# Performance work log

Measured on AMD Instinct MI355X. Metric: run time of the kernel, lower is better.

The kernel has to match this reference:

```python
import jax, jax.numpy as jnp
import numpy as np

B, N = 16, 1024
NT = 3            # atom types
NPT = 6           # pair types = NT*(NT+1)//2


def setup_inputs() -> dict:
    key = jax.random.key(0)
    ks = jax.random.split(key, 8)
    types = jax.random.randint(ks[0], (B, N), 0, NT, dtype=jnp.int32)
    n_atoms = jax.random.randint(ks[1], (B,), N // 2, N + 1, dtype=jnp.int32)
    # interatomic distances in a physically plausible range [1.5, 5.5)
    distances = 1.5 + 4.0 * jax.random.uniform(ks[2], (B, N, N), dtype=jnp.float32)
    # pair type index from (ti, tj) using combinations_with_replacement ordering
    ti = types[:, :, None]
    tj = types[:, None, :]
    lo = jnp.minimum(ti, tj)
    hi = jnp.maximum(ti, tj)
    pair_types = (lo * (2 * NT - lo + 1) // 2 + (hi - lo)).astype(jnp.int32)
    # per-pair-type potential params [a, b, r0] and density params [xi, q, r0]
    phi_params = jnp.stack([
        0.5 + jax.random.uniform(ks[3], (NPT,)),          # a
        1.0 + jax.random.uniform(ks[4], (NPT,)),          # b
        2.0 + jax.random.uniform(ks[5], (NPT,)),          # r0
    ], axis=-1).astype(jnp.float32)
    rho_params = jnp.stack([
        0.5 + jax.random.uniform(ks[6], (NPT,)),          # xi
        1.0 + jax.random.uniform(ks[7], (NPT,)),          # q
        2.0 + jax.random.uniform(jax.random.fold_in(key, 9), (NPT,)),  # r0
    ], axis=-1).astype(jnp.float32)
    emb_params = jnp.stack([
        0.5 + jax.random.uniform(jax.random.fold_in(key, 10), (NT,)),  # A (sqrt embedding)
        0.1 * jax.random.normal(jax.random.fold_in(key, 11), (NT,)),   # offset
    ], axis=-1).astype(jnp.float32)
    return {"types": types, "n_atoms": n_atoms, "distances": distances,
            "pair_types": pair_types, "phi_params": phi_params,
            "rho_params": rho_params, "emb_params": emb_params}


def reference(types, n_atoms, distances, pair_types, phi_params, rho_params, emb_params):
    # masks emulating raggedness: valid atoms and valid (i != j) pairs
    idx = jnp.arange(N)
    atom_mask = idx[None, :] < n_atoms[:, None]                      # [B, N]
    pair_mask = (atom_mask[:, :, None] & atom_mask[:, None, :]
                 & ~jnp.eye(N, dtype=bool)[None])                    # [B, N, N]

    # per-pair-type routed potential and density (branchless 'where' method)
    pp = phi_params[pair_types]                                      # [B, N, N, 3]
    phi = pp[..., 0] * jnp.exp(-pp[..., 1] * (distances - pp[..., 2]))
    rp = rho_params[pair_types]
    rho = rp[..., 0] * jnp.exp(-rp[..., 1] * (distances - rp[..., 2]))
    phi = jnp.where(pair_mask, phi, 0.0)
    rho = jnp.where(pair_mask, rho, 0.0)

    # scatter/reduce over neighbors -> per-atom quantities
    sum_rho = jnp.sum(rho * rho, axis=-1)                            # [B, N]
    sum_phi = jnp.sum(phi, axis=-1)                                  # [B, N]
    sum_rho = jnp.maximum(sum_rho, 1e-30)

    # per-atom-type embedding F(|x|) + offset
    A = emb_params[types, 0]
    off = emb_params[types, 1]
    emb = -A * jnp.sqrt(jnp.abs(sum_rho)) + off

    atomic_energies = jnp.where(atom_mask, sum_phi + emb, 0.0)       # [B, N]
    energy = jnp.sum(atomic_energies, axis=-1, keepdims=True)        # [B, 1]
    energy_per_atom = energy / n_atoms[:, None].astype(energy.dtype)
    return energy_per_atom
```

## Files before the change

### kernel.cpp

```cpp
#include <hip/hip_runtime.h>

#define NN 1024
#define BB 16
#define NTY 3

__global__ __launch_bounds__(256) void eam_rows(
    const int* __restrict__ types, const int* __restrict__ n_atoms,
    const float* __restrict__ distances,
    const float* __restrict__ phi_params, const float* __restrict__ rho_params,
    const float* __restrict__ emb_params, float* __restrict__ blk_part)
{
    __shared__ int4   s_types4[NN / 4];
    __shared__ float4 s_tbl[NTY * NTY];
    __shared__ float  s_rowe[8];

    const int tid = threadIdx.x;
    const int b  = blockIdx.y;
    const int bx = blockIdx.x;

    s_types4[tid] = ((const int4*)(types + b * NN))[tid];

    if (tid < NTY * NTY) {
        const int ti = tid / NTY, tj = tid % NTY;
        const int lo = min(ti, tj), hi = max(ti, tj);
        const int pt = lo * (2 * NTY - lo + 1) / 2 + (hi - lo);
        const float p0 = phi_params[pt * 3 + 0];
        const float p1 = phi_params[pt * 3 + 1];
        const float p2 = phi_params[pt * 3 + 2];
        const float r0 = rho_params[pt * 3 + 0];
        const float r1 = rho_params[pt * 3 + 1];
        const float r2 = rho_params[pt * 3 + 2];
        const float LOG2E = 1.44269504088896f;
        const float ra = r0 * __expf(r1 * r2);
        s_tbl[tid] = make_float4(p0 * __expf(p1 * p2), -p1 * LOG2E,
                                 ra * ra, -2.0f * r1 * LOG2E);
    }
    __syncthreads();

    const int lane = tid & 63;
    const int wave = tid >> 6;
    const int na = n_atoms[b];
    const bool p2 = na > 512;
    const bool p3 = na > 768;
    const int* s_types = (const int*)s_types4;

#pragma unroll
    for (int rr = 0; rr < 2; ++rr) {
        const int i = bx + (wave * 2 + rr) * 128;
        float rowE = 0.f;
        if (i < na) {
            const int ti = s_types[i];
            const float4* drow =
                (const float4*)(distances + ((size_t)(b * NN + i)) * NN);
            float4 v0 = drow[lane];
            float4 v1 = drow[64 + lane];
            float4 v2 = make_float4(0.f, 0.f, 0.f, 0.f);
            float4 v3 = make_float4(0.f, 0.f, 0.f, 0.f);
            if (p2) v2 = drow[128 + lane];
            if (p3) v3 = drow[192 + lane];

            float sph = 0.f, srh = 0.f;

#define EAM_EL(E, DD, TT, JB)                                                 \
            {                                                                 \
                const float4 prm = s_tbl[ti * NTY + (TT)];                    \
                float phi  = prm.x * __builtin_amdgcn_exp2f(prm.y * (DD));    \
                float rho2 = prm.z * __builtin_amdgcn_exp2f(prm.w * (DD));    \
                const int j = (JB) + (E);                                     \
                if (j >= na || j == i) { phi = 0.f; rho2 = 0.f; }             \
                sph += phi;                                                   \
                srh += rho2;                                                  \
            }
#define EAM_PASS(P, V)                                                        \
            {                                                                 \
                const int c4 = (P) * 64 + lane;                               \
                const int4 tj4 = s_types4[c4];                                \
                const int jb = c4 * 4;                                        \
                EAM_EL(0, (V).x, tj4.x, jb)                                   \
                EAM_EL(1, (V).y, tj4.y, jb)                                   \
                EAM_EL(2, (V).z, tj4.z, jb)                                   \
                EAM_EL(3, (V).w, tj4.w, jb)                                   \
            }
            EAM_PASS(0, v0)
            EAM_PASS(1, v1)
            if (p2) EAM_PASS(2, v2)
            if (p3) EAM_PASS(3, v3)
#undef EAM_PASS
#undef EAM_EL

#pragma unroll
            for (int o = 32; o > 0; o >>= 1) {
                sph += __shfl_xor(sph, o, 64);
                srh += __shfl_xor(srh, o, 64);
            }
            const float A   = emb_params[ti * 2 + 0];
            const float off = emb_params[ti * 2 + 1];
            rowE = sph + (-A * sqrtf(fmaxf(srh, 1e-30f)) + off);
        }
        if (lane == 0) s_rowe[wave * 2 + rr] = rowE;
    }
    __syncthreads();

    if (tid == 0) {
        float s = 0.f;
#pragma unroll
        for (int k = 0; k < 8; ++k) s += s_rowe[k];
        blk_part[b * 128 + bx] = s;
    }
}

__global__ __launch_bounds__(64) void eam_reduce(
    const float* __restrict__ blk_part, const int* __restrict__ n_atoms,
    float* __restrict__ out)
{
    const int b = blockIdx.x;
    const int lane = threadIdx.x;
    float s = blk_part[b * 128 + lane] + blk_part[b * 128 + 64 + lane];
#pragma unroll
    for (int o = 32; o > 0; o >>= 1) s += __shfl_xor(s, o, 64);
    if (lane == 0) out[b] = s / (float)n_atoms[b];
}

extern "C" void kernel_launch(void* const* d_in, const int* in_sizes, int n_in,
                              void* d_out, int out_size, void* d_ws, size_t ws_size,
                              hipStream_t stream) {
    const int*   types      = (const int*)d_in[0];
    const int*   n_atoms    = (const int*)d_in[1];
    const float* distances  = (const float*)d_in[2];
    const float* phi_params = (const float*)d_in[4];
    const float* rho_params = (const float*)d_in[5];
    const float* emb_params = (const float*)d_in[6];

    float* blk_part = (float*)d_ws;

    eam_rows<<<dim3(128, BB), 256, 0, stream>>>(
        types, n_atoms, distances, phi_params, rho_params, emb_params, blk_part);
    eam_reduce<<<BB, 64, 0, stream>>>(blk_part, n_atoms, (float*)d_out);
}
```

Measured before the change: 19.96 us.

## Fuse final reduction via atomics, interleave two rows, drop per-element diagonal mask

Removes the second reduce kernel by having each block atomically add its scaled partial sum into the output, which is zeroed with a memset first. Each wave now loads both of its rows up front and processes them together, so the loads overlap and the type-table lookup is shared. The per-element j==i check is replaced by subtracting the diagonal term at the end, and j>=na masking is applied only in the last pass. Risks include nondeterministic float atomic ordering, an added memset on the stream, and cancellation error from subtracting the diagonal term.

```diff
diff --git a/kernel.cpp b/kernel.cpp
--- a/kernel.cpp
+++ b/kernel.cpp
@@ -8,7 +8,7 @@
     const int* __restrict__ types, const int* __restrict__ n_atoms,
     const float* __restrict__ distances,
     const float* __restrict__ phi_params, const float* __restrict__ rho_params,
-    const float* __restrict__ emb_params, float* __restrict__ blk_part)
+    const float* __restrict__ emb_params, float* __restrict__ out)
 {
     __shared__ int4   s_types4[NN / 4];
     __shared__ float4 s_tbl[NTY * NTY];
@@ -44,60 +44,105 @@
     const bool p3 = na > 768;
     const int* s_types = (const int*)s_types4;
 
-#pragma unroll
-    for (int rr = 0; rr < 2; ++rr) {
-        const int i = bx + (wave * 2 + rr) * 128;
-        float rowE = 0.f;
-        if (i < na) {
-            const int ti = s_types[i];
-            const float4* drow =
-                (const float4*)(distances + ((size_t)(b * NN + i)) * NN);
-            float4 v0 = drow[lane];
-            float4 v1 = drow[64 + lane];
-            float4 v2 = make_float4(0.f, 0.f, 0.f, 0.f);
-            float4 v3 = make_float4(0.f, 0.f, 0.f, 0.f);
-            if (p2) v2 = drow[128 + lane];
-            if (p3) v3 = drow[192 + lane];
+    const int iA = bx + wave * 256;
+    const int iB = iA + 128;
+    const bool vA = iA < na;
+    const bool vB = iB < na;
 
-            float sph = 0.f, srh = 0.f;
+    const float4 z4 = make_float4(0.f, 0.f, 0.f, 0.f);
+    float4 a0 = z4, a1 = z4, a2 = z4, a3 = z4;
+    float4 b0 = z4, b1 = z4, b2 = z4, b3 = z4;
+    float dAii = 0.f, dBii = 0.f;
+    int tiA = 0, tiB = 0;
 
-#define EAM_EL(E, DD, TT, JB)                                                 \
-            {                                                                 \
-                const float4 prm = s_tbl[ti * NTY + (TT)];                    \
-                float phi  = prm.x * __builtin_amdgcn_exp2f(prm.y * (DD));    \
-                float rho2 = prm.z * __builtin_amdgcn_exp2f(prm.w * (DD));    \
-                const int j = (JB) + (E);                                     \
-                if (j >= na || j == i) { phi = 0.f; rho2 = 0.f; }             \
-                sph += phi;                                                   \
-                srh += rho2;                                                  \
-            }
-#define EAM_PASS(P, V)                                                        \
-            {                                                                 \
-                const int c4 = (P) * 64 + lane;                               \
-                const int4 tj4 = s_types4[c4];                                \
-                const int jb = c4 * 4;                                        \
-                EAM_EL(0, (V).x, tj4.x, jb)                                   \
-                EAM_EL(1, (V).y, tj4.y, jb)                                   \
-                EAM_EL(2, (V).z, tj4.z, jb)                                   \
-                EAM_EL(3, (V).w, tj4.w, jb)                                   \
-            }
-            EAM_PASS(0, v0)
-            EAM_PASS(1, v1)
-            if (p2) EAM_PASS(2, v2)
-            if (p3) EAM_PASS(3, v3)
+    if (vA) {
+        tiA = s_types[iA];
+        const float4* rA = (const float4*)(distances + ((size_t)(b * NN + iA)) * NN);
+        a0 = rA[lane];
+        a1 = rA[64 + lane];
+        if (p2) a2 = rA[128 + lane];
+        if (p3) a3 = rA[192 + lane];
+        dAii = ((const float*)rA)[iA];
+    }
+    if (vB) {
+        tiB = s_types[iB];
+        const float4* rB = (const float4*)(distances + ((size_t)(b * NN + iB)) * NN);
+        b0 = rB[lane];
+        b1 = rB[64 + lane];
+        if (p2) b2 = rB[128 + lane];
+        if (p3) b3 = rB[192 + lane];
+        dBii = ((const float*)rB)[iB];
+    }
+
+    float sphA = 0.f, srhA = 0.f, sphB = 0.f, srhB = 0.f;
+    const int tiA3 = tiA * NTY, tiB3 = tiB * NTY;
+
+#define EAM_EL(E, DA, DB, TT, MASKED, JB)                                     \
+    {                                                                         \
+        const int tj = (TT);                                                  \
+        const float4 pA = s_tbl[tiA3 + tj];                                   \
+        const float4 pB = s_tbl[tiB3 + tj];                                   \
+        float phA = pA.x * __builtin_amdgcn_exp2f(pA.y * (DA));               \
+        float rhA = pA.z * __builtin_amdgcn_exp2f(pA.w * (DA));               \
+        float phB = pB.x * __builtin_amdgcn_exp2f(pB.y * (DB));               \
+        float rhB = pB.z * __builtin_amdgcn_exp2f(pB.w * (DB));               \
+        if (MASKED) {                                                         \
+            const int j = (JB) + (E);                                         \
+            if (j >= na) { phA = 0.f; rhA = 0.f; phB = 0.f; rhB = 0.f; }      \
+        }                                                                     \
+        sphA += phA; srhA += rhA; sphB += phB; srhB += rhB;                   \
+    }
+#define EAM_PASS(P, VA, VB, MASKED)                                           \
+    {                                                                         \
+        const int c4 = (P) * 64 + lane;                                       \
+        const int4 tj4 = s_types4[c4];                                        \
+        const int jb = c4 * 4;                                                \
+        EAM_EL(0, (VA).x, (VB).x, tj4.x, MASKED, jb)                          \
+        EAM_EL(1, (VA).y, (VB).y, tj4.y, MASKED, jb)                          \
+        EAM_EL(2, (VA).z, (VB).z, tj4.z, MASKED, jb)                          \
+        EAM_EL(3, (VA).w, (VB).w, tj4.w, MASKED, jb)                          \
+    }
+    EAM_PASS(0, a0, b0, false)
+    EAM_PASS(1, a1, b1, false)
+    if (p3) {
+        EAM_PASS(2, a2, b2, false)
+        EAM_PASS(3, a3, b3, true)
+    } else if (p2) {
+        EAM_PASS(2, a2, b2, true)
+    }
 #undef EAM_PASS
 #undef EAM_EL
 
 #pragma unroll
-            for (int o = 32; o > 0; o >>= 1) {
-                sph += __shfl_xor(sph, o, 64);
-                srh += __shfl_xor(srh, o, 64);
-            }
-            const float A   = emb_params[ti * 2 + 0];
-            const float off = emb_params[ti * 2 + 1];
-            rowE = sph + (-A * sqrtf(fmaxf(srh, 1e-30f)) + off);
+    for (int o = 32; o > 0; o >>= 1) {
+        sphA += __shfl_xor(sphA, o, 64);
+        srhA += __shfl_xor(srhA, o, 64);
+        sphB += __shfl_xor(sphB, o, 64);
+        srhB += __shfl_xor(srhB, o, 64);
+    }
+
+    if (lane == 0) {
+        float eA = 0.f, eB = 0.f;
+        if (vA) {
+            const float4 pd = s_tbl[tiA3 + tiA];
+            const float phid = pd.x * __builtin_amdgcn_exp2f(pd.y * dAii);
+            const float rhid = pd.z * __builtin_amdgcn_exp2f(pd.w * dAii);
+            const float A   = emb_params[tiA * 2 + 0];
+            const float off = emb_params[tiA * 2 + 1];
+            eA = (sphA - phid) +
+                 (-A * sqrtf(fmaxf(srhA - rhid, 1e-30f)) + off);
         }
-        if (lane == 0) s_rowe[wave * 2 + rr] = rowE;
+        if (vB) {
+            const float4 pd = s_tbl[tiB3 + tiB];
+            const float phid = pd.x * __builtin_amdgcn_exp2f(pd.y * dBii);
+            const float rhid = pd.z * __builtin_amdgcn_exp2f(pd.w * dBii);
+            const float A   = emb_params[tiB * 2 + 0];
+            const float off = emb_params[tiB * 2 + 1];
+            eB = (sphB - phid) +
+                 (-A * sqrtf(fmaxf(srhB - rhid, 1e-30f)) + off);
+        }
+        s_rowe[wave * 2 + 0] = eA;
+        s_rowe[wave * 2 + 1] = eB;
     }
     __syncthreads();
 
@@ -105,20 +150,8 @@
         float s = 0.f;
 #pragma unroll
         for (int k = 0; k < 8; ++k) s += s_rowe[k];
-        blk_part[b * 128 + bx] = s;
+        atomicAdd(&out[b], s / (float)na);
     }
-}
-
-__global__ __launch_bounds__(64) void eam_reduce(
-    const float* __restrict__ blk_part, const int* __restrict__ n_atoms,
-    float* __restrict__ out)
-{
-    const int b = blockIdx.x;
-    const int lane = threadIdx.x;
-    float s = blk_part[b * 128 + lane] + blk_part[b * 128 + 64 + lane];
-#pragma unroll
-    for (int o = 32; o > 0; o >>= 1) s += __shfl_xor(s, o, 64);
-    if (lane == 0) out[b] = s / (float)n_atoms[b];
 }
 
 extern "C" void kernel_launch(void* const* d_in, const int* in_sizes, int n_in,
@@ -131,9 +164,9 @@
     const float* rho_params = (const float*)d_in[5];
     const float* emb_params = (const float*)d_in[6];
 
-    float* blk_part = (float*)d_ws;
+    hipMemsetAsync(d_out, 0, out_size * sizeof(float), stream);
 
     eam_rows<<<dim3(128, BB), 256, 0, stream>>>(
-        types, n_atoms, distances, phi_params, rho_params, emb_params, blk_part);
-    eam_reduce<<<BB, 64, 0, stream>>>(blk_part, n_atoms, (float*)d_out);
+        types, n_atoms, distances, phi_params, rho_params, emb_params,
+        (float*)d_out);
 }
```

New measurement: 41.78 us. +109.3%, slower.
